# Optimization experiments

Hardware: AMD Instinct MI355X
Metric: run time of the kernel (lower is better)

Reference implementation:

```python
import jax, jax.numpy as jnp
import numpy as np
import math

N = 50000        # nodes
E = 800000       # edges (avg degree 16)
F_IN = 128
F_OUT = 64


def setup_inputs() -> dict:
    key = jax.random.key(0)
    k = jax.random.split(key, 7)
    stdv = 1.0 / math.sqrt(F_OUT)
    x = jax.random.normal(k[0], (N, F_IN), dtype=jnp.float32)
    t = jax.random.uniform(k[1], (N,), dtype=jnp.float32)
    src = jax.random.randint(k[2], (E,), 0, N, dtype=jnp.int64)
    dst = jax.random.randint(k[3], (E,), 0, N, dtype=jnp.int64)
    # sparse adjacency values (e.g. normalized adjacency weights)
    edge_vals = jax.random.uniform(k[4], (E,), dtype=jnp.float32)
    weight = jax.random.uniform(k[5], (F_IN, F_OUT), dtype=jnp.float32,
                                minval=-stdv, maxval=stdv)
    bias = jax.random.uniform(k[6], (F_OUT,), dtype=jnp.float32,
                              minval=-stdv, maxval=stdv)
    return {"x": x, "t": t, "src": src, "dst": dst,
            "edge_vals": edge_vals, "weight": weight, "bias": bias}


def reference(x, t, src, dst, edge_vals, weight, bias):
    # support = (X @ W) * t[:, None]   -- dense GEMM + per-row scale
    support = (x @ weight) * t[:, None]                 # [N, F_OUT]
    # spmm(adj, support): gather rows at src, scale by edge value, reduce by dst
    msgs = support[src] * edge_vals[:, None]            # [E, F_OUT]
    out = jax.ops.segment_sum(msgs, dst, num_segments=N)  # [N, F_OUT]
    return out + bias
```

## Files before the change

### kernel.cpp

```cpp
#include <hip/hip_runtime.h>
#include <hip/hip_bf16.h>

#define FIN 128
#define FOUT 64
#define TILE_ROWS 64

#define EPB 2048
#define NPB 32
#define NBUK_MAX 1600
#define CAP 768

#define OFF_CUR   6400000
#define OFF_OVFC  6406400
#define OFF_TMP   6406464
#define OFF_OVF   16236864

typedef short bf16x8 __attribute__((ext_vector_type(8)));
typedef float f32x4  __attribute__((ext_vector_type(4)));

__device__ inline ushort f32_to_bf16_rne(float f) {
    unsigned u = __float_as_uint(f);
    u += 0x7FFFu + ((u >> 16) & 1u);
    return (ushort)(u >> 16);
}
__device__ inline float bf16_to_f32(ushort h) {
    return __uint_as_float((unsigned)h << 16);
}

union __align__(16) K1Sh {
    ushort wt[FOUT * FIN];
    struct { int h[NBUK_MAX]; int c[NBUK_MAX]; } sc;
};

__global__ __launch_bounds__(256) void gemm_scatter_kernel(
    const float* __restrict__ x, const float* __restrict__ t,
    const float* __restrict__ W, ushort* __restrict__ support, int N,
    const int* __restrict__ src, const int* __restrict__ dst,
    const float* __restrict__ ev, int* __restrict__ cur,
    int2* __restrict__ tmp, int* __restrict__ ovfc, int4* __restrict__ ovf,
    int E, int SBP, int NBUK, int GB)
{
    __shared__ K1Sh sh;
    const int tid = threadIdx.x;

    if (blockIdx.x >= (unsigned)GB) {
        const int chunk = blockIdx.x - GB;
        const int e0    = chunk * EPB;

        for (int i = tid; i < NBUK; i += 256) sh.sc.h[i] = 0;
        __syncthreads();

        for (int i = tid; i < EPB; i += 256) {
            int e = e0 + i;
            if (e < E) atomicAdd(&sh.sc.h[dst[e] >> 5], 1);
        }
        __syncthreads();

        for (int j = tid; j < NBUK; j += 256) {
            int hj = sh.sc.h[j];
            if (hj) sh.sc.c[j] = atomicAdd(&cur[j], hj);
        }
        __syncthreads();

        for (int i = tid; i < EPB; i += 256) {
            int e = e0 + i;
            if (e < E) {
                int d = dst[e];
                int j = d >> 5;
                int s = atomicAdd(&sh.sc.c[j], 1);
                int2 rec = make_int2(src[e] | ((d & (NPB - 1)) << 16),
                                     __float_as_int(ev[e]));
                if (s < CAP) {
                    tmp[(size_t)j * CAP + s] = rec;
                } else {
                    int o = atomicAdd(ovfc, 1);
                    if (o < E) ovf[o] = make_int4(rec.x, rec.y, j, 0);
                }
            }
        }
        return;
    }

    const int gb   = blockIdx.x;
    const int lane = tid & 63;
    const int w    = tid >> 6;
    const int ln   = lane & 15;
    const int q    = lane >> 4;
    const int rowb = gb * TILE_ROWS + w * 16;
    const int arow = rowb + ln;

    for (int idx = tid; idx < FIN * FOUT; idx += 256) {
        int k = idx >> 6;
        int n = idx & 63;
        sh.wt[n * FIN + (k ^ ((n & 7) << 3))] = f32_to_bf16_rne(W[idx]);
    }
    __syncthreads();

    f32x4 acc[4];
    #pragma unroll
    for (int nt = 0; nt < 4; ++nt)
        #pragma unroll
        for (int r = 0; r < 4; ++r) acc[nt][r] = 0.f;

    const bool aok = (arow < N);
    const float* xrow = &x[(size_t)arow * FIN];

    #pragma unroll
    for (int kc = 0; kc < 4; ++kc) {
        float xs[8];
        #pragma unroll
        for (int j = 0; j < 8; ++j) xs[j] = 0.f;
        if (aok) {
            float4 x0 = *(const float4*)&xrow[kc * 32 + q * 8];
            float4 x1 = *(const float4*)&xrow[kc * 32 + q * 8 + 4];
            xs[0] = x0.x; xs[1] = x0.y; xs[2] = x0.z; xs[3] = x0.w;
            xs[4] = x1.x; xs[5] = x1.y; xs[6] = x1.z; xs[7] = x1.w;
        }
        bf16x8 a;
        #pragma unroll
        for (int j = 0; j < 8; ++j) a[j] = (short)f32_to_bf16_rne(xs[j]);

        const int k0 = kc * 32 + q * 8;
        #pragma unroll
        for (int nt = 0; nt < 4; ++nt) {
            bf16x8 b = *(const bf16x8*)
                &sh.wt[(nt * 16 + ln) * FIN + (k0 ^ ((ln & 7) << 3))];
            acc[nt] = __builtin_amdgcn_mfma_f32_16x16x32_bf16(a, b, acc[nt], 0, 0, 0);
        }
    }

    #pragma unroll
    for (int reg = 0; reg < 4; ++reg) {
        int r = rowb + q * 4 + reg;
        if (r < N) {
            float tv = t[r];
            #pragma unroll
            for (int nt = 0; nt < 4; ++nt)
                support[(size_t)r * FOUT + nt * 16 + ln] =
                    f32_to_bf16_rne(acc[nt][reg] * tv);
        }
    }
}

__global__ __launch_bounds__(256) void bucket_gather_kernel(
    const int* __restrict__ curg, const int2* __restrict__ tmp,
    const ushort* __restrict__ support, const float* __restrict__ bias,
    float* __restrict__ out, const int* __restrict__ ovfc,
    const int4* __restrict__ ovf, int E, int N, int NBUK)
{
    __shared__ int2 raw[CAP];
    __shared__ int2 sorted[CAP];
    __shared__ int  cnt[NPB];
    __shared__ int  starts[NPB + 1];
    __shared__ int  cur[NPB];
    __shared__ int  novs;

    const int tid   = threadIdx.x;
    const int w     = tid >> 6;
    const int lane  = tid & 63;
    const int B     = blockIdx.x;
    const int node0 = B * NPB;

    const int base   = B * CAP;
    const int tot    = curg[B];
    const int placed = (tot < CAP) ? tot : CAP;

    if (tid < NPB) cnt[tid] = 0;
    __syncthreads();

    for (int i = tid; i < placed; i += 256) {
        int2 r = tmp[base + i];
        raw[i] = r;
        atomicAdd(&cnt[(r.x >> 16) & (NPB - 1)], 1);
    }
    __syncthreads();

    if (tid < 64) {
        int v   = (tid < NPB) ? cnt[tid] : 0;
        int val = v;
        #pragma unroll
        for (int d = 1; d < NPB; d <<= 1) {
            int n = __shfl_up(val, d);
            if (tid >= d) val += n;
        }
        if (tid < NPB) {
            starts[tid] = val - v;
            cur[tid]    = val - v;
        }
        if (tid == 0) starts[NPB] = placed;
    }
    __syncthreads();

    for (int i = tid; i < placed; i += 256) {
        int2 r  = raw[i];
        int pos = atomicAdd(&cur[(r.x >> 16) & (NPB - 1)], 1);
        sorted[pos] = r;
    }
    __syncthreads();

    const int fl = lane & 15;
    const int g  = lane >> 4;
    const float4 bv4 = *(const float4*)&bias[fl * 4];

    for (int nn = 0; nn < 8; ++nn) {
        const int nl = w * 8 + nn;
        const int rb = starts[nl];
        const int re = starts[nl + 1];

        float a0 = 0.f, a1 = 0.f, a2 = 0.f, a3 = 0.f;
        for (int i = rb + g; i < re; i += 4) {
            int2 r = sorted[i];
            uint2 u = *(const uint2*)
                &support[(size_t)(r.x & 0xFFFF) * FOUT + fl * 4];
            float wg = __int_as_float(r.y);
            a0 += bf16_to_f32((ushort)(u.x & 0xFFFFu)) * wg;
            a1 += bf16_to_f32((ushort)(u.x >> 16)) * wg;
            a2 += bf16_to_f32((ushort)(u.y & 0xFFFFu)) * wg;
            a3 += bf16_to_f32((ushort)(u.y >> 16)) * wg;
        }
        #pragma unroll
        for (int d = 16; d < 64; d <<= 1) {
            a0 += __shfl_xor(a0, d);
            a1 += __shfl_xor(a1, d);
            a2 += __shfl_xor(a2, d);
            a3 += __shfl_xor(a3, d);
        }
        const int node = node0 + nl;
        if (g == 0 && node < N) {
            float4 o;
            o.x = a0 + bv4.x; o.y = a1 + bv4.y;
            o.z = a2 + bv4.z; o.w = a3 + bv4.w;
            *(float4*)&out[(size_t)node * FOUT + fl * 4] = o;
        }
    }

    __syncthreads();
    if (tid == 0) novs = *ovfc;
    __syncthreads();
    int nov = novs;
    if (nov > 0) {
        if (nov > E) nov = E;
        __threadfence();
        for (int k = w; k < nov; k += 4) {
            int4 r = ovf[k];
            if (r.z == B) {
                int node = node0 + ((r.x >> 16) & (NPB - 1));
                if (node < N) {
                    float v = bf16_to_f32(
                        support[(size_t)(r.x & 0xFFFF) * FOUT + lane]);
                    atomicAdd(&out[(size_t)node * FOUT + lane],
                              v * __int_as_float(r.y));
                }
            }
        }
    }
}

extern "C" void kernel_launch(void* const* d_in, const int* in_sizes, int n_in,
                              void* d_out, int out_size, void* d_ws, size_t ws_size,
                              hipStream_t stream) {
    const float* x    = (const float*)d_in[0];
    const float* t    = (const float*)d_in[1];
    const int*   src  = (const int*)d_in[2];
    const int*   dst  = (const int*)d_in[3];
    const float* ev   = (const float*)d_in[4];
    const float* W    = (const float*)d_in[5];
    const float* bias = (const float*)d_in[6];
    float* out = (float*)d_out;

    const int N = in_sizes[1];
    const int E = in_sizes[2];

    char*   ws      = (char*)d_ws;
    ushort* support = (ushort*)ws;
    int*    cur     = (int*)(ws + OFF_CUR);
    int*    ovfc    = (int*)(ws + OFF_OVFC);
    int2*   tmp     = (int2*)(ws + OFF_TMP);
    int4*   ovf     = (int4*)(ws + OFF_OVF);

    const int GB   = (N + TILE_ROWS - 1) / TILE_ROWS;
    const int SBP  = (E + EPB - 1) / EPB;
    const int NBUK = (N + NPB - 1) / NPB;

    hipMemsetAsync(ws + OFF_CUR, 0, OFF_TMP - OFF_CUR, stream);

    gemm_scatter_kernel<<<GB + SBP, 256, 0, stream>>>(
        x, t, W, support, N, src, dst, ev, cur, tmp, ovfc, ovf,
        E, SBP, NBUK, GB);

    bucket_gather_kernel<<<NBUK, 256, 0, stream>>>(
        cur, tmp, support, bias, out, ovfc, ovf, E, N, NBUK);
}
```

Measured before the change: 132.5 us.

## Double GEMM tile rows, schedule scatter blocks first, vectorize W load, drop raw LDS copy

The fused GEMM/scatter kernel now places the edge-scatter blocks at the low block indices so they are dispatched first. Each GEMM wave computes two 16-row M tiles, so every W fragment read from LDS feeds twice as many MFMAs and half as many blocks stage W. W is loaded with float4 reads. The gather kernel drops its raw LDS staging buffer and rereads records from global memory, which is likely cache-resident, to cut LDS use and raise occupancy. The cost is more registers per GEMM thread and a second global read of each record.

```diff
diff --git a/kernel.cpp b/kernel.cpp
--- a/kernel.cpp
+++ b/kernel.cpp
@@ -3,7 +3,7 @@
 
 #define FIN 128
 #define FOUT 64
-#define TILE_ROWS 64
+#define TILE_ROWS 128
 
 #define EPB 2048
 #define NPB 32
@@ -43,8 +43,8 @@
     __shared__ K1Sh sh;
     const int tid = threadIdx.x;
 
-    if (blockIdx.x >= (unsigned)GB) {
-        const int chunk = blockIdx.x - GB;
+    if (blockIdx.x < (unsigned)SBP) {
+        const int chunk = blockIdx.x;
         const int e0    = chunk * EPB;
 
         for (int i = tid; i < NBUK; i += 256) sh.sc.h[i] = 0;
@@ -81,63 +81,91 @@
         return;
     }
 
-    const int gb   = blockIdx.x;
+    const int gb   = blockIdx.x - SBP;
     const int lane = tid & 63;
     const int w    = tid >> 6;
     const int ln   = lane & 15;
     const int q    = lane >> 4;
-    const int rowb = gb * TILE_ROWS + w * 16;
-    const int arow = rowb + ln;
-
-    for (int idx = tid; idx < FIN * FOUT; idx += 256) {
-        int k = idx >> 6;
-        int n = idx & 63;
-        sh.wt[n * FIN + (k ^ ((n & 7) << 3))] = f32_to_bf16_rne(W[idx]);
-    }
-    __syncthreads();
-
-    f32x4 acc[4];
+    const int rowb = gb * TILE_ROWS + w * 32;
+
+    for (int it = 0; it < 8; ++it) {
+        int eidx = (tid + it * 256) * 4;
+        float4 wv = *(const float4*)&W[eidx];
+        int k  = eidx >> 6;
+        int n0 = eidx & 63;
+        sh.wt[(n0 + 0) * FIN + (k ^ (((n0 + 0) & 7) << 3))] = f32_to_bf16_rne(wv.x);
+        sh.wt[(n0 + 1) * FIN + (k ^ (((n0 + 1) & 7) << 3))] = f32_to_bf16_rne(wv.y);
+        sh.wt[(n0 + 2) * FIN + (k ^ (((n0 + 2) & 7) << 3))] = f32_to_bf16_rne(wv.z);
+        sh.wt[(n0 + 3) * FIN + (k ^ (((n0 + 3) & 7) << 3))] = f32_to_bf16_rne(wv.w);
+    }
+    __syncthreads();
+
+    f32x4 acc[2][4];
     #pragma unroll
-    for (int nt = 0; nt < 4; ++nt)
-        #pragma unroll
-        for (int r = 0; r < 4; ++r) acc[nt][r] = 0.f;
-
-    const bool aok = (arow < N);
-    const float* xrow = &x[(size_t)arow * FIN];
+    for (int mt = 0; mt < 2; ++mt)
+        #pragma unroll
+        for (int nt = 0; nt < 4; ++nt)
+            #pragma unroll
+            for (int r = 0; r < 4; ++r) acc[mt][nt][r] = 0.f;
+
+    const int arow0 = rowb + ln;
+    const int arow1 = rowb + 16 + ln;
+    const bool aok0 = (arow0 < N);
+    const bool aok1 = (arow1 < N);
+    const float* xrow0 = &x[(size_t)arow0 * FIN];
+    const float* xrow1 = &x[(size_t)arow1 * FIN];
 
     #pragma unroll
     for (int kc = 0; kc < 4; ++kc) {
-        float xs[8];
-        #pragma unroll
-        for (int j = 0; j < 8; ++j) xs[j] = 0.f;
-        if (aok) {
-            float4 x0 = *(const float4*)&xrow[kc * 32 + q * 8];
-            float4 x1 = *(const float4*)&xrow[kc * 32 + q * 8 + 4];
-            xs[0] = x0.x; xs[1] = x0.y; xs[2] = x0.z; xs[3] = x0.w;
-            xs[4] = x1.x; xs[5] = x1.y; xs[6] = x1.z; xs[7] = x1.w;
-        }
-        bf16x8 a;
-        #pragma unroll
-        for (int j = 0; j < 8; ++j) a[j] = (short)f32_to_bf16_rne(xs[j]);
-
         const int k0 = kc * 32 + q * 8;
+        bf16x8 a0, a1;
+        {
+            float xs[8];
+            #pragma unroll
+            for (int j = 0; j < 8; ++j) xs[j] = 0.f;
+            if (aok0) {
+                float4 v0 = *(const float4*)&xrow0[k0];
+                float4 v1 = *(const float4*)&xrow0[k0 + 4];
+                xs[0] = v0.x; xs[1] = v0.y; xs[2] = v0.z; xs[3] = v0.w;
+                xs[4] = v1.x; xs[5] = v1.y; xs[6] = v1.z; xs[7] = v1.w;
+            }
+            #pragma unroll
+            for (int j = 0; j < 8; ++j) a0[j] = (short)f32_to_bf16_rne(xs[j]);
+        }
+        {
+            float xs[8];
+            #pragma unroll
+            for (int j = 0; j < 8; ++j) xs[j] = 0.f;
+            if (aok1) {
+                float4 v0 = *(const float4*)&xrow1[k0];
+                float4 v1 = *(const float4*)&xrow1[k0 + 4];
+                xs[0] = v0.x; xs[1] = v0.y; xs[2] = v0.z; xs[3] = v0.w;
+                xs[4] = v1.x; xs[5] = v1.y; xs[6] = v1.z; xs[7] = v1.w;
+            }
+            #pragma unroll
+            for (int j = 0; j < 8; ++j) a1[j] = (short)f32_to_bf16_rne(xs[j]);
+        }
         #pragma unroll
         for (int nt = 0; nt < 4; ++nt) {
             bf16x8 b = *(const bf16x8*)
                 &sh.wt[(nt * 16 + ln) * FIN + (k0 ^ ((ln & 7) << 3))];
-            acc[nt] = __builtin_amdgcn_mfma_f32_16x16x32_bf16(a, b, acc[nt], 0, 0, 0);
+            acc[0][nt] = __builtin_amdgcn_mfma_f32_16x16x32_bf16(a0, b, acc[0][nt], 0, 0, 0);
+            acc[1][nt] = __builtin_amdgcn_mfma_f32_16x16x32_bf16(a1, b, acc[1][nt], 0, 0, 0);
         }
     }
 
     #pragma unroll
-    for (int reg = 0; reg < 4; ++reg) {
-        int r = rowb + q * 4 + reg;
-        if (r < N) {
-            float tv = t[r];
-            #pragma unroll
-            for (int nt = 0; nt < 4; ++nt)
-                support[(size_t)r * FOUT + nt * 16 + ln] =
-                    f32_to_bf16_rne(acc[nt][reg] * tv);
+    for (int mt = 0; mt < 2; ++mt) {
+        #pragma unroll
+        for (int reg = 0; reg < 4; ++reg) {
+            int r = rowb + mt * 16 + q * 4 + reg;
+            if (r < N) {
+                float tv = t[r];
+                #pragma unroll
+                for (int nt = 0; nt < 4; ++nt)
+                    support[(size_t)r * FOUT + nt * 16 + ln] =
+                        f32_to_bf16_rne(acc[mt][nt][reg] * tv);
+            }
         }
     }
 }
@@ -148,7 +176,6 @@
     float* __restrict__ out, const int* __restrict__ ovfc,
     const int4* __restrict__ ovf, int E, int N, int NBUK)
 {
-    __shared__ int2 raw[CAP];
     __shared__ int2 sorted[CAP];
     __shared__ int  cnt[NPB];
     __shared__ int  starts[NPB + 1];
@@ -170,7 +197,6 @@
 
     for (int i = tid; i < placed; i += 256) {
         int2 r = tmp[base + i];
-        raw[i] = r;
         atomicAdd(&cnt[(r.x >> 16) & (NPB - 1)], 1);
     }
     __syncthreads();
@@ -192,7 +218,7 @@
     __syncthreads();
 
     for (int i = tid; i < placed; i += 256) {
-        int2 r  = raw[i];
+        int2 r  = tmp[base + i];
         int pos = atomicAdd(&cur[(r.x >> 16) & (NPB - 1)], 1);
         sorted[pos] = r;
     }
@@ -284,7 +310,7 @@
 
     hipMemsetAsync(ws + OFF_CUR, 0, OFF_TMP - OFF_CUR, stream);
 
-    gemm_scatter_kernel<<<GB + SBP, 256, 0, stream>>>(
+    gemm_scatter_kernel<<<SBP + GB, 256, 0, stream>>>(
         x, t, W, support, N, src, dst, ev, cur, tmp, ovfc, ovf,
         E, SBP, NBUK, GB);
 
```

Result: slower. 137.9 us (+4.1%).
